# Kernel tuning notes

Measured on AMD Instinct MI355X. Metric: run time of the kernel, lower is better.

## Reference

```python
import jax, jax.numpy as jnp
import numpy as np
from jax import lax

B, T, C, H, HOR = 64, 2048, 64, 256, 96
BETA, THR = 0.9, 1.0


def setup_inputs() -> dict:
    key = jax.random.key(0)
    ks = jax.random.split(key, 10)
    s = lambda *sh: 1.0 / np.sqrt(sh[-1])
    return {
        "x": jax.random.normal(ks[0], (B, T, C), jnp.float32),
        "snn_w": jax.random.uniform(ks[1], (H, C), jnp.float32, -s(C), s(C)),
        "snn_b": jax.random.uniform(ks[2], (H,), jnp.float32, -s(C), s(C)),
        "gru_wih": jax.random.uniform(ks[3], (3 * H, C + H), jnp.float32, -s(H), s(H)),
        "gru_whh": jax.random.uniform(ks[4], (3 * H, H), jnp.float32, -s(H), s(H)),
        "gru_bih": jax.random.uniform(ks[5], (3 * H,), jnp.float32, -s(H), s(H)),
        "gru_bhh": jax.random.uniform(ks[6], (3 * H,), jnp.float32, -s(H), s(H)),
        "head_w": jax.random.uniform(ks[7], (HOR, H), jnp.float32, -s(H), s(H)),
        "head_b": jax.random.uniform(ks[8], (HOR,), jnp.float32, -s(H), s(H)),
    }


@jax.custom_vjp
def spike(x):
    return (x > 0).astype(x.dtype)

def _spike_fwd(x):
    return spike(x), x

def _spike_bwd(x, g):
    # snntorch ATan surrogate, alpha=2: grad = 1 / (1 + (pi*x)^2)
    return (g / (1.0 + (jnp.pi * x) ** 2),)

spike.defvjp(_spike_fwd, _spike_bwd)


def reference(x, snn_w, snn_b, gru_wih, gru_whh, gru_bih, gru_bhh, head_w, head_b):
    # Batched SNN input current across all timesteps: [B,T,H]
    cur = jnp.einsum("btc,hc->bth", x, snn_w) + snn_b

    def lif_step(mem, i_t):
        # reset computed from previous mem, detached (snntorch mem_reset)
        reset = lax.stop_gradient((mem > THR).astype(mem.dtype))
        mem_new = BETA * mem + i_t - reset * THR
        spk = spike(mem_new - THR)
        return mem_new, spk

    mem0 = jnp.zeros((B, H), x.dtype)
    _, spks = lax.scan(lif_step, mem0, cur.transpose(1, 0, 2))  # [T,B,H]

    h_comb = jnp.concatenate([x, spks.transpose(1, 0, 2)], axis=-1)  # [B,T,C+H]

    # GRU: precompute input gates for all timesteps
    gx = jnp.einsum("btc,gc->btg", h_comb, gru_wih) + gru_bih  # [B,T,3H]

    def gru_step(h, gx_t):
        gh = h @ gru_whh.T + gru_bhh
        xr, xz, xn = jnp.split(gx_t, 3, axis=-1)
        hr, hz, hn = jnp.split(gh, 3, axis=-1)
        r = jax.nn.sigmoid(xr + hr)
        z = jax.nn.sigmoid(xz + hz)
        n = jnp.tanh(xn + r * hn)
        h_new = (1.0 - z) * n + z * h
        return h_new, None

    h0 = jnp.zeros((B, H), x.dtype)
    hT, _ = lax.scan(gru_step, h0, gx.transpose(1, 0, 2))

    return hT @ head_w.T + head_b  # [B, HOR]
```

## Files before the change

### kernel.cpp

```cpp
#include <hip/hip_runtime.h>
#include <cstdint>
#include <cstddef>

#define B_   64
#define T_   2048
#define C_   64
#define H_   256
#define G3_  768
#define HOR_ 96

typedef _Float16 h2 __attribute__((ext_vector_type(2)));
typedef _Float16 h8 __attribute__((ext_vector_type(8)));
typedef _Float16 f16x8 __attribute__((ext_vector_type(8)));
typedef float f32x4 __attribute__((ext_vector_type(4)));

#define K1_TT 128
__global__ __launch_bounds__(256) void k_cur(const float* __restrict__ x,
                                             const float* __restrict__ w,
                                             const float* __restrict__ bias,
                                             float* __restrict__ cur,
                                             int* __restrict__ flags) {
  __shared__ float xs[K1_TT * C_];
  const int b = blockIdx.x;
  const int t0 = blockIdx.y * K1_TT;
  const int tid = threadIdx.x;

  if (b == 0 && blockIdx.y == 0) {
#pragma unroll
    for (int i = 0; i < 4; i++) flags[tid + i * 256] = 0;
  }

  const float4* xsrc = (const float4*)(x + ((size_t)b * T_ + t0) * C_);
  float4* xdst = (float4*)xs;
#pragma unroll
  for (int i = 0; i < (K1_TT * C_ / 4) / 256; i++)
    xdst[tid + i * 256] = xsrc[tid + i * 256];

  float wr[C_];
  const float4* wp = (const float4*)(w + (size_t)tid * C_);
#pragma unroll
  for (int q = 0; q < C_ / 4; q++) {
    float4 v = wp[q];
    wr[4 * q + 0] = v.x; wr[4 * q + 1] = v.y;
    wr[4 * q + 2] = v.z; wr[4 * q + 3] = v.w;
  }
  const float bb = bias[tid];
  __syncthreads();

  for (int t = 0; t < K1_TT; t++) {
    const float4* xrow = (const float4*)(xs + t * C_);
    float a0 = 0.f, a1 = 0.f;
#pragma unroll
    for (int q = 0; q < C_ / 4; q += 2) {
      float4 v0 = xrow[q];
      float4 v1 = xrow[q + 1];
      a0 += wr[4 * q + 0] * v0.x + wr[4 * q + 1] * v0.y +
            wr[4 * q + 2] * v0.z + wr[4 * q + 3] * v0.w;
      a1 += wr[4 * q + 4] * v1.x + wr[4 * q + 5] * v1.y +
            wr[4 * q + 6] * v1.z + wr[4 * q + 7] * v1.w;
    }
    cur[((size_t)b * T_ + t0 + t) * H_ + tid] = a0 + a1 + bb;
  }
}

__global__ __launch_bounds__(64) void k_lif(const float* __restrict__ cur,
                                            unsigned char* __restrict__ spk) {
  const int b = blockIdx.x >> 2;
  const int h = ((blockIdx.x & 3) << 6) + threadIdx.x;
  const float* cp = cur + (size_t)b * T_ * H_ + h;
  unsigned char* sp = spk + (size_t)b * T_ * H_ + h;
  float mem = 0.f;
#pragma unroll 64
  for (int t = 0; t < T_; t++) {
    float c = cp[(size_t)t * H_];
    float reset = (mem > 1.0f) ? 1.0f : 0.0f;
    mem = 0.9f * mem + c - reset;
    sp[(size_t)t * H_] = (mem > 1.0f) ? (unsigned char)1 : (unsigned char)0;
  }
}

#define GM 128
#define GN 128
#define AKP 40
#define CTP 136
#define DQ_ (0.0625f / (127.0f * 127.0f))
__global__ __launch_bounds__(256) void k_fused(
    const float* __restrict__ x, const unsigned char* __restrict__ spk,
    const float* __restrict__ wih, const float* __restrict__ bih,
    _Float16* __restrict__ gx, const float* __restrict__ whh,
    const float* __restrict__ bhh, const float* __restrict__ head_w,
    const float* __restrict__ head_b, float* __restrict__ out,
    int* __restrict__ flags) {
  alignas(16) __shared__ _Float16 Ah[GM * AKP];
  alignas(16) __shared__ _Float16 Bh[GN * AKP];
  alignas(16) __shared__ _Float16 Ct[GM * CTP];
  alignas(16) __shared__ int hq[2][64];
  __shared__ float hbuf32[H_];

  const int tid = threadIdx.x;
  const int lane = tid & 63;

  if (blockIdx.x >= 64) {
    const int pidx = blockIdx.x - 64;
    const int bb = pidx / 3;
    const int pp = pidx - bb * 3;
    const int wave = tid >> 6;
    const int ln = lane & 15;
    const int qd = lane >> 4;
    const int wm = (wave & 1) * 64;
    const int wn = ((wave >> 1) & 1) * 64;

    for (int mt = 0; mt < 16; mt++) {
      const int m0 = bb * 2048 + mt * 128;
      for (int nh = 0; nh < 2; nh++) {
        const int n0 = pp * 256 + nh * 128;
        f32x4 acc[4][4] = {};
        for (int kc = 0; kc < 10; kc++) {
          const int k0 = kc * 32;
          if (k0 < 64) {
#pragma unroll
            for (int i = 0; i < 4; i++) {
              int idx = tid + i * 256;
              int r = idx >> 3;
              int c4 = (idx & 7) * 4;
              float4 v = *(const float4*)(x + (size_t)(m0 + r) * C_ + k0 + c4);
              h2 lo, hi;
              lo.x = (_Float16)v.x; lo.y = (_Float16)v.y;
              hi.x = (_Float16)v.z; hi.y = (_Float16)v.w;
              h2* d = (h2*)&Ah[r * AKP + c4];
              d[0] = lo; d[1] = hi;
            }
          } else {
#pragma unroll
            for (int i = 0; i < 4; i++) {
              int idx = tid + i * 256;
              int r = idx >> 3;
              int c4 = (idx & 7) * 4;
              uchar4 u = *(const uchar4*)(spk + (size_t)(m0 + r) * H_ + (k0 - 64) + c4);
              h2 lo, hi;
              lo.x = (_Float16)(int)u.x; lo.y = (_Float16)(int)u.y;
              hi.x = (_Float16)(int)u.z; hi.y = (_Float16)(int)u.w;
              h2* d = (h2*)&Ah[r * AKP + c4];
              d[0] = lo; d[1] = hi;
            }
          }
#pragma unroll
          for (int i = 0; i < 4; i++) {
            int idx = tid + i * 256;
            int r = idx >> 3;
            int c4 = (idx & 7) * 4;
            float4 v = *(const float4*)(wih + (size_t)(n0 + r) * 320 + k0 + c4);
            h2 lo, hi;
            lo.x = (_Float16)v.x; lo.y = (_Float16)v.y;
            hi.x = (_Float16)v.z; hi.y = (_Float16)v.w;
            h2* d = (h2*)&Bh[r * AKP + c4];
            d[0] = lo; d[1] = hi;
          }
          __syncthreads();
          {
            f16x8 a[4], bbf[4];
#pragma unroll
            for (int mtl = 0; mtl < 4; mtl++)
              a[mtl] = *(const f16x8*)&Ah[(wm + mtl * 16 + ln) * AKP + qd * 8];
#pragma unroll
            for (int nt = 0; nt < 4; nt++)
              bbf[nt] = *(const f16x8*)&Bh[(wn + nt * 16 + ln) * AKP + qd * 8];
#pragma unroll
            for (int mtl = 0; mtl < 4; mtl++)
#pragma unroll
              for (int nt = 0; nt < 4; nt++)
                acc[mtl][nt] = __builtin_amdgcn_mfma_f32_16x16x32_f16(
                    a[mtl], bbf[nt], acc[mtl][nt], 0, 0, 0);
          }
          __syncthreads();
        }
        {
          float bias[4];
#pragma unroll
          for (int nt = 0; nt < 4; nt++) bias[nt] = bih[n0 + wn + nt * 16 + ln];
#pragma unroll
          for (int mtl = 0; mtl < 4; mtl++)
#pragma unroll
            for (int nt = 0; nt < 4; nt++) {
              int n = wn + nt * 16 + ln;
#pragma unroll
              for (int r = 0; r < 4; r++) {
                int m = wm + mtl * 16 + qd * 4 + r;
                Ct[m * CTP + n] = (_Float16)(acc[mtl][nt][r] + bias[nt]);
              }
            }
        }
        __syncthreads();
#pragma unroll
        for (int i = 0; i < 8; i++) {
          int idx = tid + i * 256;
          int r = idx >> 4;
          int c = (idx & 15) * 8;
          *(h8*)(gx + (size_t)(m0 + r) * G3_ + n0 + c) = *(const h8*)&Ct[r * CTP + c];
        }
        __syncthreads();
      }
      if (tid == 0)
        __hip_atomic_fetch_add(&flags[bb * 16 + mt], 1, __ATOMIC_RELEASE,
                               __HIP_MEMORY_SCOPE_AGENT);
    }
    return;
  }

  const int b = blockIdx.x;
  const int j = tid;

  int wr[64], wz[64], wn2[64];
  {
    const float qs = 2032.0f;
    const float4* p0 = (const float4*)(whh + (size_t)j * H_);
    const float4* p1 = (const float4*)(whh + (size_t)(H_ + j) * H_);
    const float4* p2 = (const float4*)(whh + (size_t)(2 * H_ + j) * H_);
#pragma unroll
    for (int q = 0; q < 64; q++) {
      float4 a = p0[q];
      wr[q] = ((int)rintf(a.x * qs) & 255) | (((int)rintf(a.y * qs) & 255) << 8) |
              (((int)rintf(a.z * qs) & 255) << 16) | (((int)rintf(a.w * qs) & 255) << 24);
      float4 c = p1[q];
      wz[q] = ((int)rintf(c.x * qs) & 255) | (((int)rintf(c.y * qs) & 255) << 8) |
              (((int)rintf(c.z * qs) & 255) << 16) | (((int)rintf(c.w * qs) & 255) << 24);
      float4 d = p2[q];
      wn2[q] = ((int)rintf(d.x * qs) & 255) | (((int)rintf(d.y * qs) & 255) << 8) |
               (((int)rintf(d.z * qs) & 255) << 16) | (((int)rintf(d.w * qs) & 255) << 24);
    }
  }
  const float br_ = bhh[j], bz_ = bhh[H_ + j], bn_ = bhh[2 * H_ + j];

  if (tid < 128) ((int*)hq)[tid] = 0;
  float hj = 0.f;
  __syncthreads();

  const _Float16* gxb = gx + (size_t)b * T_ * G3_;
  int p = 0;
  for (int mt = 0; mt < 16; mt++) {
    if (tid == 0) {
      while (__hip_atomic_load(&flags[b * 16 + mt], __ATOMIC_ACQUIRE,
                               __HIP_MEMORY_SCOPE_AGENT) < 3)
        __builtin_amdgcn_s_sleep(8);
    }
    __syncthreads();

    const _Float16* gc = gxb + (size_t)mt * 128 * G3_;
    _Float16 pr = gc[j], pz = gc[H_ + j], pn = gc[2 * H_ + j];

    for (int tt = 0; tt < 128; tt++) {
      _Float16 npr = pr, npz = pz, npn = pn;
      if (tt < 127) {
        const _Float16* g = gc + (size_t)(tt + 1) * G3_;
        npr = g[j]; npz = g[H_ + j]; npn = g[2 * H_ + j];
      }
      __builtin_amdgcn_sched_barrier(0);

      float xr = (float)pr, xz = (float)pz, xn = (float)pn;

      const int4* hb4 = (const int4*)hq[p];
      int ar0 = 0, ar1 = 0, az0 = 0, az1 = 0, an0 = 0, an1 = 0;
      int4 c0 = hb4[0], c1 = hb4[1], c2 = hb4[2], c3 = hb4[3];
#pragma unroll
      for (int g = 0; g < 4; g++) {
        int4 n0, n1, n2, n3;
        if (g < 3) {
          n0 = hb4[g * 4 + 4]; n1 = hb4[g * 4 + 5];
          n2 = hb4[g * 4 + 6]; n3 = hb4[g * 4 + 7];
        }
#pragma unroll
        for (int cc = 0; cc < 4; cc++) {
          int4 hv = (cc == 0) ? c0 : (cc == 1) ? c1 : (cc == 2) ? c2 : c3;
#pragma unroll
          for (int i = 0; i < 4; i++) {
            int h4 = (i == 0) ? hv.x : (i == 1) ? hv.y : (i == 2) ? hv.z : hv.w;
            int wi = g * 16 + cc * 4 + i;
            if (wi & 1) {
              ar1 = __builtin_amdgcn_sdot4(wr[wi], h4, ar1, false);
              az1 = __builtin_amdgcn_sdot4(wz[wi], h4, az1, false);
              an1 = __builtin_amdgcn_sdot4(wn2[wi], h4, an1, false);
            } else {
              ar0 = __builtin_amdgcn_sdot4(wr[wi], h4, ar0, false);
              az0 = __builtin_amdgcn_sdot4(wz[wi], h4, az0, false);
              an0 = __builtin_amdgcn_sdot4(wn2[wi], h4, an0, false);
            }
          }
        }
        __builtin_amdgcn_sched_barrier(2 | 4 | 16 | 32 | 64);
        if (g < 3) { c0 = n0; c1 = n1; c2 = n2; c3 = n3; }
      }
      int ar = ar0 + ar1, az = az0 + az1, an = an0 + an1;

      float r = 1.f / (1.f + __expf(-(xr + (float)ar * DQ_ + br_)));
      float z = 1.f / (1.f + __expf(-(xz + (float)az * DQ_ + bz_)));
      float pre = xn + r * ((float)an * DQ_ + bn_);
      float e = __expf(2.f * pre);
      float n = 1.f - 2.f / (e + 1.f);
      hj = (1.f - z) * n + z * hj;

      ((char*)hq[p ^ 1])[j] = (char)(int)rintf(hj * 127.0f);
      pr = npr; pz = npz; pn = npn;
      p ^= 1;
      __syncthreads();
    }
  }

  hbuf32[j] = hj;
  __syncthreads();

  if (tid < HOR_) {
    const float4* hw = (const float4*)(head_w + (size_t)tid * H_);
    const float4* hv4 = (const float4*)hbuf32;
    float acc = head_b[tid];
#pragma unroll
    for (int q = 0; q < H_ / 4; q++) {
      float4 w4 = hw[q];
      float4 v4 = hv4[q];
      acc += w4.x * v4.x + w4.y * v4.y + w4.z * v4.z + w4.w * v4.w;
    }
    out[(size_t)b * HOR_ + tid] = acc;
  }
}

extern "C" void kernel_launch(void* const* d_in, const int* in_sizes, int n_in,
                              void* d_out, int out_size, void* d_ws, size_t ws_size,
                              hipStream_t stream) {
  const float* x      = (const float*)d_in[0];
  const float* snn_w  = (const float*)d_in[1];
  const float* snn_b  = (const float*)d_in[2];
  const float* wih    = (const float*)d_in[3];
  const float* whh    = (const float*)d_in[4];
  const float* bih    = (const float*)d_in[5];
  const float* bhh    = (const float*)d_in[6];
  const float* head_w = (const float*)d_in[7];
  const float* head_b = (const float*)d_in[8];
  float* out = (float*)d_out;

  char* ws = (char*)d_ws;
  _Float16* gx = (_Float16*)ws;
  float* cur = (float*)ws;
  unsigned char* spk = (unsigned char*)(ws + (size_t)201326592);
  int* flags = (int*)(ws + (size_t)234881024);

  k_cur<<<dim3(B_, T_ / K1_TT), 256, 0, stream>>>(x, snn_w, snn_b, cur, flags);
  k_lif<<<dim3(256), 64, 0, stream>>>(cur, spk);
  k_fused<<<dim3(256), 256, 0, stream>>>(x, spk, wih, bih, gx, whh, bhh,
                                         head_w, head_b, out, flags);
}
```

Measured before the change: 2.234 ms.

## Fuse SNN current and LIF scan into gate-GEMM producer blocks with flag pipelining

Removes the separate k_cur and k_lif kernels. The pp==0 producer block of each batch now computes the SNN input current and runs the LIF recurrence per 128-step tile, writing spikes, and signals a per-tile flag. The sibling GEMM producers wait on that flag before building gx, and the GRU consumer waits for the combined flag count. This drops the full fp32 cur round trip through memory and the separate serial LIF pass, letting spike generation overlap with the GEMM and the GRU. The cost is more serial work on one producer block per batch, which might delay the gx tiles.

```diff
diff --git a/kernel.cpp b/kernel.cpp
--- a/kernel.cpp
+++ b/kernel.cpp
@@ -14,69 +14,9 @@
 typedef _Float16 f16x8 __attribute__((ext_vector_type(8)));
 typedef float f32x4 __attribute__((ext_vector_type(4)));
 
-#define K1_TT 128
-__global__ __launch_bounds__(256) void k_cur(const float* __restrict__ x,
-                                             const float* __restrict__ w,
-                                             const float* __restrict__ bias,
-                                             float* __restrict__ cur,
-                                             int* __restrict__ flags) {
-  __shared__ float xs[K1_TT * C_];
-  const int b = blockIdx.x;
-  const int t0 = blockIdx.y * K1_TT;
-  const int tid = threadIdx.x;
-
-  if (b == 0 && blockIdx.y == 0) {
-#pragma unroll
-    for (int i = 0; i < 4; i++) flags[tid + i * 256] = 0;
-  }
-
-  const float4* xsrc = (const float4*)(x + ((size_t)b * T_ + t0) * C_);
-  float4* xdst = (float4*)xs;
-#pragma unroll
-  for (int i = 0; i < (K1_TT * C_ / 4) / 256; i++)
-    xdst[tid + i * 256] = xsrc[tid + i * 256];
-
-  float wr[C_];
-  const float4* wp = (const float4*)(w + (size_t)tid * C_);
-#pragma unroll
-  for (int q = 0; q < C_ / 4; q++) {
-    float4 v = wp[q];
-    wr[4 * q + 0] = v.x; wr[4 * q + 1] = v.y;
-    wr[4 * q + 2] = v.z; wr[4 * q + 3] = v.w;
-  }
-  const float bb = bias[tid];
-  __syncthreads();
-
-  for (int t = 0; t < K1_TT; t++) {
-    const float4* xrow = (const float4*)(xs + t * C_);
-    float a0 = 0.f, a1 = 0.f;
-#pragma unroll
-    for (int q = 0; q < C_ / 4; q += 2) {
-      float4 v0 = xrow[q];
-      float4 v1 = xrow[q + 1];
-      a0 += wr[4 * q + 0] * v0.x + wr[4 * q + 1] * v0.y +
-            wr[4 * q + 2] * v0.z + wr[4 * q + 3] * v0.w;
-      a1 += wr[4 * q + 4] * v1.x + wr[4 * q + 5] * v1.y +
-            wr[4 * q + 6] * v1.z + wr[4 * q + 7] * v1.w;
-    }
-    cur[((size_t)b * T_ + t0 + t) * H_ + tid] = a0 + a1 + bb;
-  }
-}
-
-__global__ __launch_bounds__(64) void k_lif(const float* __restrict__ cur,
-                                            unsigned char* __restrict__ spk) {
-  const int b = blockIdx.x >> 2;
-  const int h = ((blockIdx.x & 3) << 6) + threadIdx.x;
-  const float* cp = cur + (size_t)b * T_ * H_ + h;
-  unsigned char* sp = spk + (size_t)b * T_ * H_ + h;
-  float mem = 0.f;
-#pragma unroll 64
-  for (int t = 0; t < T_; t++) {
-    float c = cp[(size_t)t * H_];
-    float reset = (mem > 1.0f) ? 1.0f : 0.0f;
-    mem = 0.9f * mem + c - reset;
-    sp[(size_t)t * H_] = (mem > 1.0f) ? (unsigned char)1 : (unsigned char)0;
-  }
+__global__ __launch_bounds__(256) void k_zero(int* __restrict__ flags) {
+#pragma unroll
+  for (int i = 0; i < 4; i++) flags[threadIdx.x + i * 256] = 0;
 }
 
 #define GM 128
@@ -85,7 +25,8 @@
 #define CTP 136
 #define DQ_ (0.0625f / (127.0f * 127.0f))
 __global__ __launch_bounds__(256) void k_fused(
-    const float* __restrict__ x, const unsigned char* __restrict__ spk,
+    const float* __restrict__ x, const float* __restrict__ snn_w,
+    const float* __restrict__ snn_b, unsigned char* __restrict__ spk,
     const float* __restrict__ wih, const float* __restrict__ bih,
     _Float16* __restrict__ gx, const float* __restrict__ whh,
     const float* __restrict__ bhh, const float* __restrict__ head_w,
@@ -110,8 +51,60 @@
     const int wm = (wave & 1) * 64;
     const int wn = ((wave >> 1) & 1) * 64;
 
+    float wsn[C_];
+    float bsn = 0.f, memv = 0.f;
+    if (pp == 0) {
+      const float4* wp = (const float4*)(snn_w + (size_t)tid * C_);
+#pragma unroll
+      for (int q = 0; q < C_ / 4; q++) {
+        float4 v = wp[q];
+        wsn[4 * q + 0] = v.x; wsn[4 * q + 1] = v.y;
+        wsn[4 * q + 2] = v.z; wsn[4 * q + 3] = v.w;
+      }
+      bsn = snn_b[tid];
+    }
+
     for (int mt = 0; mt < 16; mt++) {
       const int m0 = bb * 2048 + mt * 128;
+
+      if (pp == 0) {
+        float* xs = (float*)Ct;
+        const float4* xsrc = (const float4*)(x + ((size_t)bb * T_ + mt * 128) * C_);
+        float4* xdst = (float4*)xs;
+#pragma unroll
+        for (int i = 0; i < 8; i++) xdst[tid + i * 256] = xsrc[tid + i * 256];
+        __syncthreads();
+        unsigned char* sp = spk + ((size_t)bb * T_ + mt * 128) * H_ + tid;
+        for (int t = 0; t < 128; t++) {
+          const float4* xrow = (const float4*)(xs + t * C_);
+          float a0 = 0.f, a1 = 0.f;
+#pragma unroll
+          for (int q = 0; q < C_ / 4; q += 2) {
+            float4 v0 = xrow[q];
+            float4 v1 = xrow[q + 1];
+            a0 += wsn[4 * q + 0] * v0.x + wsn[4 * q + 1] * v0.y +
+                  wsn[4 * q + 2] * v0.z + wsn[4 * q + 3] * v0.w;
+            a1 += wsn[4 * q + 4] * v1.x + wsn[4 * q + 5] * v1.y +
+                  wsn[4 * q + 6] * v1.z + wsn[4 * q + 7] * v1.w;
+          }
+          float c = a0 + a1 + bsn;
+          float reset = (memv > 1.0f) ? 1.0f : 0.0f;
+          memv = 0.9f * memv + c - reset;
+          sp[(size_t)t * H_] = (memv > 1.0f) ? (unsigned char)1 : (unsigned char)0;
+        }
+        __syncthreads();
+        if (tid == 0)
+          __hip_atomic_fetch_add(&flags[bb * 16 + mt], 1, __ATOMIC_RELEASE,
+                                 __HIP_MEMORY_SCOPE_AGENT);
+      }
+
+      if (tid == 0) {
+        while ((__hip_atomic_load(&flags[bb * 16 + mt], __ATOMIC_ACQUIRE,
+                                  __HIP_MEMORY_SCOPE_AGENT) & 7) < 1)
+          __builtin_amdgcn_s_sleep(8);
+      }
+      __syncthreads();
+
       for (int nh = 0; nh < 2; nh++) {
         const int n0 = pp * 256 + nh * 128;
         f32x4 acc[4][4] = {};
@@ -201,7 +194,7 @@
         __syncthreads();
       }
       if (tid == 0)
-        __hip_atomic_fetch_add(&flags[bb * 16 + mt], 1, __ATOMIC_RELEASE,
+        __hip_atomic_fetch_add(&flags[bb * 16 + mt], 8, __ATOMIC_RELEASE,
                                __HIP_MEMORY_SCOPE_AGENT);
     }
     return;
@@ -240,7 +233,7 @@
   for (int mt = 0; mt < 16; mt++) {
     if (tid == 0) {
       while (__hip_atomic_load(&flags[b * 16 + mt], __ATOMIC_ACQUIRE,
-                               __HIP_MEMORY_SCOPE_AGENT) < 3)
+                               __HIP_MEMORY_SCOPE_AGENT) < 25)
         __builtin_amdgcn_s_sleep(8);
     }
     __syncthreads();
@@ -338,12 +331,10 @@
 
   char* ws = (char*)d_ws;
   _Float16* gx = (_Float16*)ws;
-  float* cur = (float*)ws;
   unsigned char* spk = (unsigned char*)(ws + (size_t)201326592);
   int* flags = (int*)(ws + (size_t)234881024);
 
-  k_cur<<<dim3(B_, T_ / K1_TT), 256, 0, stream>>>(x, snn_w, snn_b, cur, flags);
-  k_lif<<<dim3(256), 64, 0, stream>>>(cur, spk);
-  k_fused<<<dim3(256), 256, 0, stream>>>(x, spk, wih, bih, gx, whh, bhh,
-                                         head_w, head_b, out, flags);
+  k_zero<<<dim3(1), 256, 0, stream>>>(flags);
+  k_fused<<<dim3(256), 256, 0, stream>>>(x, snn_w, snn_b, spk, wih, bih, gx,
+                                         whh, bhh, head_w, head_b, out, flags);
 }
```

Result: faster. 1.973 ms (-11.7%).
